# Optimization experiments

Measured on AMD Instinct MI355X. Metric: run time of the kernel, lower is better.

## Reference

```python
import math
import jax, jax.numpy as jnp
import numpy as np

LMAX = 2


def _cg_complex(j1, m1, j2, m2, j3, m3):
    # Standard (Racah) Clebsch-Gordan coefficient <j1 m1 j2 m2 | j3 m3> for integer l.
    if m1 + m2 != m3 or j3 < abs(j1 - j2) or j3 > j1 + j2:
        return 0.0
    f = math.factorial
    pre = math.sqrt((2 * j3 + 1) * f(j3 + j1 - j2) * f(j3 - j1 + j2) * f(j1 + j2 - j3) / f(j1 + j2 + j3 + 1))
    pre *= math.sqrt(f(j3 + m3) * f(j3 - m3) * f(j1 - m1) * f(j1 + m1) * f(j2 - m2) * f(j2 + m2))
    kmin = max(0, j2 - j3 - m1, j1 + m2 - j3)
    kmax = min(j1 + j2 - j3, j1 - m1, j2 + m2)
    s = 0.0
    for k in range(kmin, kmax + 1):
        s += (-1.0) ** k / (f(k) * f(j1 + j2 - j3 - k) * f(j1 - m1 - k) * f(j2 + m2 - k) * f(j3 - j2 + m1 + k) * f(j3 - j1 - m2 + k))
    return pre * s


def _u_matrix(l):
    # Unitary map from complex SH (Condon-Shortley) to real SH, rows = real mu, cols = complex m.
    U = np.zeros((2 * l + 1, 2 * l + 1), dtype=np.complex128)
    U[l, l] = 1.0
    isq2 = 1.0 / math.sqrt(2.0)
    for m in range(1, l + 1):
        U[l + m, l - m] = isq2
        U[l + m, l + m] = ((-1.0) ** m) * isq2
        U[l - m, l - m] = 1j * isq2
        U[l - m, l + m] = -1j * ((-1.0) ** m) * isq2
    return U


def _real_clebsch_gordan(lmax):
    # Dense real-SH CG tensor over combined s=(l,m) indices, shape [S,S,S], S=(lmax+1)^2.
    S = (lmax + 1) ** 2
    cg = np.zeros((S, S, S))
    for l1 in range(lmax + 1):
        for l2 in range(lmax + 1):
            for l3 in range(abs(l1 - l2), min(lmax, l1 + l2) + 1):
                blk = np.zeros((2 * l1 + 1, 2 * l2 + 1, 2 * l3 + 1))
                for i1, m1 in enumerate(range(-l1, l1 + 1)):
                    for i2, m2 in enumerate(range(-l2, l2 + 1)):
                        for i3, m3 in enumerate(range(-l3, l3 + 1)):
                            blk[i1, i2, i3] = _cg_complex(l1, m1, l2, m2, l3, m3)
                U1, U2, U3 = _u_matrix(l1), _u_matrix(l2), _u_matrix(l3)
                r = np.einsum('am,bn,co,mno->abc', U1, U2, U3.conj(), blk.astype(np.complex128))
                r = r.real if (l1 + l2 + l3) % 2 == 0 else r.imag  # parity-dependent real part
                cg[l1 * l1:(l1 + 1) ** 2, l2 * l2:(l2 + 1) ** 2, l3 * l3:(l3 + 1) ** 2] = r
    return cg


def _sparse_cg(lmax):
    cg = _real_clebsch_gordan(lmax)
    i1, i2, i3 = np.nonzero(np.abs(cg) > 1e-10)
    vals = cg[i1, i2, i3].astype(np.float32)
    widx = np.floor(np.sqrt(i3.astype(np.float64))).astype(np.int32)  # l of output combined index
    return vals, i1.astype(np.int32), i2.astype(np.int32), i3.astype(np.int32), widx


def _spherical_harmonics_l2(d):
    # Real SH up to l=2, 'component' normalization (|x|=1 assumed). Order: (l,m) = (0,0),(1,-1),(1,0),(1,1),(2,-2..2).
    x, y, z = d[..., 0], d[..., 1], d[..., 2]
    s3, s5, s15 = math.sqrt(3.0), math.sqrt(5.0), math.sqrt(15.0)
    return jnp.stack([
        jnp.ones_like(x),
        s3 * y, s3 * z, s3 * x,
        s15 * x * y, s15 * y * z, 0.5 * s5 * (3.0 * z * z - 1.0), s15 * x * z, 0.5 * s15 * (x * x - y * y),
    ], axis=-1)


def setup_inputs():
    N_ATOMS, N_EDGES, N_BASIS, N_RADIAL = 1200, 12000, 128, 20
    S = (LMAX + 1) ** 2
    key = jax.random.key(0)
    ks = jax.random.split(key, 8)
    vals, i1, i2, i3, widx = _sparse_cg(LMAX)
    return {
        'x': jax.random.normal(ks[0], (N_ATOMS, S, N_BASIS), jnp.float32),
        'radial_ij': jax.random.uniform(ks[1], (N_EDGES, N_RADIAL), jnp.float32),
        'dir_ij': jax.random.normal(ks[2], (N_EDGES, 3), jnp.float32),
        'cutoff_ij': jax.random.uniform(ks[3], (N_EDGES, 1), jnp.float32),
        'W_filter': jax.random.normal(ks[6], (N_RADIAL, N_BASIS * (LMAX + 1)), jnp.float32) / math.sqrt(N_RADIAL),
        'b_filter': jnp.zeros((N_BASIS * (LMAX + 1),), jnp.float32),
        'cg_vals': jnp.asarray(vals),
        'idx_i': jax.random.randint(ks[4], (N_EDGES,), 0, N_ATOMS),
        'idx_j': jax.random.randint(ks[5], (N_EDGES,), 0, N_ATOMS),
        'cg_idx_in1': jnp.asarray(i1),
        'cg_idx_in2': jnp.asarray(i2),
        'cg_idx_out': jnp.asarray(i3),
        'w_idx': jnp.asarray(widx),
    }


def reference(x, radial_ij, dir_ij, cutoff_ij, W_filter, b_filter, cg_vals,
              idx_i, idx_j, cg_idx_in1, cg_idx_in2, cg_idx_out, w_idx):
    n_atoms, S, F = x.shape
    E = dir_ij.shape[0]
    d = dir_ij / jnp.linalg.norm(dir_ij, axis=-1, keepdims=True)
    Y = _spherical_harmonics_l2(d)                        # [E, S]
    Wij = (radial_ij @ W_filter + b_filter) * cutoff_ij   # [E, (lmax+1)*F]
    Wij = Wij.reshape(E, LMAX + 1, F)                     # per-l radial filter
    xj = x[idx_j]                                         # [E, S, F] neighbor features
    # Sparse CG tensor-product contraction over combined (l,m) indices.
    v = (Y[:, cg_idx_in2, None] * cg_vals[None, :, None]
         * Wij[:, w_idx, :] * xj[:, cg_idx_in1, :])       # [E, n_cg, F]
    yij = jnp.zeros((E, S, F), v.dtype).at[:, cg_idx_out, :].add(v)
    return jax.ops.segment_sum(yij, idx_i, num_segments=n_atoms)
```

## Files before the change

kernel.cpp:

```cpp
#include <hip/hip_runtime.h>
#include <math.h>


#define S9     9
#define MROW   12
#define NF     128
#define NRAD   20
#define CEDGE  4
#define MAXA   2048

__device__ inline float2 f2fma(float a, float2 b, float2 c) {
    return make_float2(fmaf(a, b.x, c.x), fmaf(a, b.y, c.y));
}

__global__ __launch_bounds__(1024) void csr_kernel(
    const int* __restrict__ idx_i, int E, int A, int max_chunks,
    int* __restrict__ offsets,
    int* __restrict__ chunk_off,
    int* __restrict__ chunk_atom,
    int* __restrict__ esorted,
    float* __restrict__ out)
{
    __shared__ int lcnt[MAXA];
    __shared__ int lcur[MAXA];
    __shared__ unsigned long long wtot[16];
    __shared__ int nch_sh;
    const int t = threadIdx.x;
    const int lane = t & 63;
    const int wid  = t >> 6;

    for (int i = t; i < A; i += 1024) lcnt[i] = 0;
    __syncthreads();
    for (int e = t; e < E; e += 1024) atomicAdd(&lcnt[idx_i[e]], 1);
    __syncthreads();

    const int i0 = 2 * t, i1 = 2 * t + 1;
    const int ca = (i0 < A) ? lcnt[i0] : 0;
    const int cb = (i1 < A) ? lcnt[i1] : 0;
    const int ka = (i0 < A) ? ((ca + CEDGE - 1) / CEDGE) : 0;
    const int kb = (i1 < A) ? ((cb + CEDGE - 1) / CEDGE) : 0;

    const unsigned long long mine =
        (unsigned long long)(unsigned)(ca + cb) |
        ((unsigned long long)(unsigned)(ka + kb) << 32);
    unsigned long long inc = mine;
    #pragma unroll
    for (int d = 1; d < 64; d <<= 1) {
        unsigned long long u = __shfl_up(inc, d);
        if (lane >= d) inc += u;
    }
    if (lane == 63) wtot[wid] = inc;
    __syncthreads();
    if (wid == 0) {
        unsigned long long w = (lane < 16) ? wtot[lane] : 0ull;
        #pragma unroll
        for (int d = 1; d < 16; d <<= 1) {
            unsigned long long u = __shfl_up(w, d);
            if (lane >= d) w += u;
        }
        if (lane < 16) wtot[lane] = w;
    }
    __syncthreads();
    const unsigned long long wpre = (wid > 0) ? wtot[wid - 1] : 0ull;
    const unsigned long long exc  = wpre + (inc - mine);

    int run  = (int)(exc & 0xffffffffull);
    int run2 = (int)(exc >> 32);
    if (i0 < A) {
        offsets[i0] = run; lcur[i0] = run; chunk_off[i0] = run2;
        for (int k = 0; k < ka; ++k) chunk_atom[run2 + k] = i0;
        run += ca; run2 += ka;
    }
    if (i1 < A) {
        offsets[i1] = run; lcur[i1] = run; chunk_off[i1] = run2;
        for (int k = 0; k < kb; ++k) chunk_atom[run2 + k] = i1;
        run += cb; run2 += kb;
    }
    if (t == 1023) {
        const unsigned long long g = wtot[15];
        offsets[A]   = (int)(g & 0xffffffffull);
        chunk_off[A] = (int)(g >> 32);
        nch_sh       = (int)(g >> 32);
    }

    const float4 z4 = make_float4(0.f, 0.f, 0.f, 0.f);
    if (i0 < A && ca == 0) {
        float4* o = (float4*)(out + (size_t)i0 * (S9 * NF));
        for (int s = 0; s < S9 * NF / 4; ++s) o[s] = z4;
    }
    if (i1 < A && cb == 0) {
        float4* o = (float4*)(out + (size_t)i1 * (S9 * NF));
        for (int s = 0; s < S9 * NF / 4; ++s) o[s] = z4;
    }
    __syncthreads();

    for (int i = nch_sh + t; i < max_chunks; i += 1024) chunk_atom[i] = -1;

    for (int e = t; e < E; e += 1024) {
        int p = atomicAdd(&lcur[idx_i[e]], 1);
        esorted[p] = e;
    }
}

__global__ __launch_bounds__(64) void so3_chunk_kernel(
    const float* __restrict__ x,
    const float* __restrict__ radial,
    const float* __restrict__ dir,
    const float* __restrict__ cutoff,
    const float* __restrict__ Wf,
    const float* __restrict__ bf,
    const float* __restrict__ cg_vals,
    const int* __restrict__ idx_j,
    const int* __restrict__ cg_i1,
    const int* __restrict__ cg_i2,
    const int* __restrict__ cg_i3,
    int ncg, int A,
    const int* __restrict__ offsets,
    const int* __restrict__ chunk_off,
    const int* __restrict__ chunk_atom,
    const int* __restrict__ esorted,
    float* __restrict__ slots,
    float* __restrict__ out,
    int use_slots)
{
    const int ch = blockIdx.x;
    const int a = chunk_atom[ch];
    if (a < 0) return;

    const int c0ch = chunk_off[a];
    const int nch  = chunk_off[a + 1] - c0ch;
    const int estart = offsets[a] + (ch - c0ch) * CEDGE;
    const int n = min(CEDGE, offsets[a + 1] - estart);

    const int t = threadIdx.x;

    __shared__ __align__(16) float M[CEDGE][MROW * S9];
    __shared__ float Ysh[CEDGE][S9];
    __shared__ float radsh[CEDGE][NRAD];
    __shared__ float cutsh[CEDGE];
    __shared__ int   jsh[CEDGE];

    {
        float4* Mz = (float4*)&M[0][0];
        const int tot4 = CEDGE * MROW * S9 / 4;
        for (int qq = t; qq < tot4; qq += 64) Mz[qq] = make_float4(0.f, 0.f, 0.f, 0.f);
    }
    if (t < CEDGE) {
        int jj = a;
        float cut = 0.f;
        if (t < n) {
            const int e = esorted[estart + t];
            jj = idx_j[e];
            cut = cutoff[e];
            float dx = dir[3 * e], dy = dir[3 * e + 1], dz = dir[3 * e + 2];
            const float inv = rsqrtf(dx * dx + dy * dy + dz * dz);
            dx *= inv; dy *= inv; dz *= inv;
            const float s3c  = 1.7320508075688772f;
            const float s5c  = 2.2360679774997896f;
            const float s15c = 3.8729833462074170f;
            Ysh[t][0] = 1.0f;
            Ysh[t][1] = s3c * dy;
            Ysh[t][2] = s3c * dz;
            Ysh[t][3] = s3c * dx;
            Ysh[t][4] = s15c * dx * dy;
            Ysh[t][5] = s15c * dy * dz;
            Ysh[t][6] = 0.5f * s5c * (3.0f * dz * dz - 1.0f);
            Ysh[t][7] = s15c * dx * dz;
            Ysh[t][8] = 0.5f * s15c * (dx * dx - dy * dy);
        }
        jsh[t] = jj;
        cutsh[t] = cut;
    }
    for (int qq = t; qq < CEDGE * NRAD; qq += 64) {
        const int c = qq / NRAD;
        const int r = qq - c * NRAD;
        radsh[c][r] = (c < n) ? radial[(size_t)esorted[estart + c] * NRAD + r] : 0.f;
    }
    __syncthreads();

    float2 w[CEDGE][3];
    {
        const float2 b0 = ((const float2*)(bf + 0 * NF))[t];
        const float2 b1 = ((const float2*)(bf + 1 * NF))[t];
        const float2 b2 = ((const float2*)(bf + 2 * NF))[t];
        #pragma unroll
        for (int c = 0; c < CEDGE; ++c) { w[c][0] = b0; w[c][1] = b1; w[c][2] = b2; }
        #pragma unroll 4
        for (int r = 0; r < NRAD; ++r) {
            const float2* wrow = (const float2*)(Wf + r * (3 * NF));
            const float2 w0 = wrow[t];
            const float2 w1 = wrow[t + 64];
            const float2 w2 = wrow[t + 128];
            #pragma unroll
            for (int c = 0; c < CEDGE; ++c) {
                const float rv = radsh[c][r];
                w[c][0] = f2fma(rv, w0, w[c][0]);
                w[c][1] = f2fma(rv, w1, w[c][1]);
                w[c][2] = f2fma(rv, w2, w[c][2]);
            }
        }
        #pragma unroll
        for (int c = 0; c < CEDGE; ++c) {
            const float cut = cutsh[c];
            w[c][0].x *= cut; w[c][0].y *= cut;
            w[c][1].x *= cut; w[c][1].y *= cut;
            w[c][2].x *= cut; w[c][2].y *= cut;
        }
    }

    {
        const int c = t >> 4;
        const int r = t & 15;
        if (c < n) {
            for (int kk = r; kk < ncg; kk += 16) {
                atomicAdd(&M[c][cg_i3[kk] * MROW + cg_i1[kk]], cg_vals[kk] * Ysh[c][cg_i2[kk]]);
            }
        }
    }
    __syncthreads();

    float2 acc[S9];
    #pragma unroll
    for (int s = 0; s < S9; ++s) acc[s] = make_float2(0.f, 0.f);

    #pragma unroll
    for (int c = 0; c < CEDGE; ++c) {
        const int j = __builtin_amdgcn_readfirstlane(jsh[c]);

        const float2* xp = (const float2*)(x + (size_t)j * (S9 * NF)) + t;
        float2 xj[S9];
        #pragma unroll
        for (int s = 0; s < S9; ++s) xj[s] = xp[s * 64];

        #pragma unroll
        for (int s3 = 0; s3 < S9; ++s3) {
            const float4* mr = (const float4*)&M[c][s3 * MROW];
            const float4 m0 = mr[0];
            const float4 m1 = mr[1];
            const float  m8 = M[c][s3 * MROW + 8];
            float2 tsum = make_float2(0.f, 0.f);
            tsum = f2fma(m0.x, xj[0], tsum);
            tsum = f2fma(m0.y, xj[1], tsum);
            tsum = f2fma(m0.z, xj[2], tsum);
            tsum = f2fma(m0.w, xj[3], tsum);
            tsum = f2fma(m1.x, xj[4], tsum);
            tsum = f2fma(m1.y, xj[5], tsum);
            tsum = f2fma(m1.z, xj[6], tsum);
            tsum = f2fma(m1.w, xj[7], tsum);
            tsum = f2fma(m8,   xj[8], tsum);
            const float2 wl = (s3 == 0) ? w[c][0] : ((s3 < 4) ? w[c][1] : w[c][2]);
            acc[s3].x = fmaf(wl.x, tsum.x, acc[s3].x);
            acc[s3].y = fmaf(wl.y, tsum.y, acc[s3].y);
        }
    }

    if (!use_slots) {
        float* op = out + (size_t)a * (S9 * NF) + 2 * t;
        #pragma unroll
        for (int s = 0; s < S9; ++s) {
            atomicAdd(&op[s * NF],     acc[s].x);
            atomicAdd(&op[s * NF + 1], acc[s].y);
        }
        return;
    }

    if (nch == 1) {
        float2* op = (float2*)(out + (size_t)a * (S9 * NF)) + t;
        #pragma unroll
        for (int s = 0; s < S9; ++s) op[s * 64] = acc[s];
    } else {
        float2* sp = (float2*)(slots + (size_t)ch * (S9 * NF)) + t;
        #pragma unroll
        for (int s = 0; s < S9; ++s) sp[s * 64] = acc[s];
    }
}

__global__ __launch_bounds__(64) void so3_reduce_kernel(
    const float* __restrict__ slots, const int* __restrict__ chunk_off,
    float* __restrict__ out)
{
    const int a = blockIdx.x;
    const int t = threadIdx.x;
    const int c0 = chunk_off[a];
    const int c1 = chunk_off[a + 1];
    if (c1 - c0 < 2) return;

    float2 acc[S9];
    #pragma unroll
    for (int s = 0; s < S9; ++s) acc[s] = make_float2(0.f, 0.f);

    for (int ch = c0; ch < c1; ++ch) {
        const float2* sp = (const float2*)(slots + (size_t)ch * (S9 * NF)) + t;
        #pragma unroll
        for (int s = 0; s < S9; ++s) {
            float2 v = sp[s * 64];
            acc[s].x += v.x; acc[s].y += v.y;
        }
    }
    float2* op = (float2*)(out + (size_t)a * (S9 * NF)) + t;
    #pragma unroll
    for (int s = 0; s < S9; ++s) op[s * 64] = acc[s];
}

extern "C" void kernel_launch(void* const* d_in, const int* in_sizes, int n_in,
                              void* d_out, int out_size, void* d_ws, size_t ws_size,
                              hipStream_t stream) {
    const float* x       = (const float*)d_in[0];
    const float* radial  = (const float*)d_in[1];
    const float* dir     = (const float*)d_in[2];
    const float* cutoff  = (const float*)d_in[3];
    const float* Wf      = (const float*)d_in[4];
    const float* bf      = (const float*)d_in[5];
    const float* cg_vals = (const float*)d_in[6];
    const int*   idx_i   = (const int*)d_in[7];
    const int*   idx_j   = (const int*)d_in[8];
    const int*   cg_i1   = (const int*)d_in[9];
    const int*   cg_i2   = (const int*)d_in[10];
    const int*   cg_i3   = (const int*)d_in[11];

    const int E   = in_sizes[7];
    const int ncg = in_sizes[6];
    const int A   = in_sizes[0] / (S9 * NF);

    const int max_chunks = E / CEDGE + A;

    int* offsets    = (int*)d_ws;
    int* chunk_off  = offsets + (A + 1);
    int* chunk_atom = chunk_off + (A + 1);
    int* esorted    = chunk_atom + max_chunks;
    size_t int_bytes = (size_t)(2 * A + 2 + max_chunks + E) * sizeof(int);
    size_t slots_off = (int_bytes + 255) & ~(size_t)255;

    size_t slots_bytes = (size_t)max_chunks * (S9 * NF) * sizeof(float);
    const int use_slots = (ws_size >= slots_off + slots_bytes) ? 1 : 0;
    float* slots = (float*)((char*)d_ws + slots_off);
    float* out   = (float*)d_out;

    if (!use_slots) {
        hipMemsetAsync(out, 0, (size_t)out_size * sizeof(float), stream);
    }

    csr_kernel<<<1, 1024, 0, stream>>>(idx_i, E, A, max_chunks,
                                       offsets, chunk_off, chunk_atom, esorted, out);

    so3_chunk_kernel<<<max_chunks, 64, 0, stream>>>(
        x, radial, dir, cutoff, Wf, bf, cg_vals, idx_j,
        cg_i1, cg_i2, cg_i3, ncg, A, offsets, chunk_off, chunk_atom, esorted,
        slots, out, use_slots);

    if (use_slots) {
        so3_reduce_kernel<<<A, 64, 0, stream>>>(slots, chunk_off, out);
    }
}
```

Baseline: 124.5 us.

## Process all edges of an atom in one block, drop chunk slots and reduce pass

Replaces the per-chunk grid (4 edges per block, partial sums written to slots, then a separate reduce kernel) with one block per atom that loops over that atom's edges in tiles of 8 and writes the output directly. The CSR build is simplified to plain offsets, and the edge sort is staged in shared memory when E fits. This removes the slot traffic, the third kernel launch and the chunk bookkeeping. In exchange the grid shrinks to A blocks of 64 threads, so parallelism falls and atoms with many edges become serial tails.

```diff
diff --git a/kernel.cpp b/kernel.cpp
--- a/kernel.cpp
+++ b/kernel.cpp
@@ -6,25 +6,22 @@
 #define MROW   12
 #define NF     128
 #define NRAD   20
-#define CEDGE  4
+#define TEDGE  8
 #define MAXA   2048
+#define EMAX   12288
 
 __device__ inline float2 f2fma(float a, float2 b, float2 c) {
     return make_float2(fmaf(a, b.x, c.x), fmaf(a, b.y, c.y));
 }
 
 __global__ __launch_bounds__(1024) void csr_kernel(
-    const int* __restrict__ idx_i, int E, int A, int max_chunks,
+    const int* __restrict__ idx_i, int E, int A,
     int* __restrict__ offsets,
-    int* __restrict__ chunk_off,
-    int* __restrict__ chunk_atom,
-    int* __restrict__ esorted,
-    float* __restrict__ out)
+    int* __restrict__ esorted)
 {
     __shared__ int lcnt[MAXA];
-    __shared__ int lcur[MAXA];
-    __shared__ unsigned long long wtot[16];
-    __shared__ int nch_sh;
+    __shared__ int wtot[16];
+    __shared__ int esh[EMAX];
     const int t = threadIdx.x;
     const int lane = t & 63;
     const int wid  = t >> 6;
@@ -37,72 +34,48 @@
     const int i0 = 2 * t, i1 = 2 * t + 1;
     const int ca = (i0 < A) ? lcnt[i0] : 0;
     const int cb = (i1 < A) ? lcnt[i1] : 0;
-    const int ka = (i0 < A) ? ((ca + CEDGE - 1) / CEDGE) : 0;
-    const int kb = (i1 < A) ? ((cb + CEDGE - 1) / CEDGE) : 0;
-
-    const unsigned long long mine =
-        (unsigned long long)(unsigned)(ca + cb) |
-        ((unsigned long long)(unsigned)(ka + kb) << 32);
-    unsigned long long inc = mine;
+    __syncthreads();
+
+    int inc = ca + cb;
     #pragma unroll
     for (int d = 1; d < 64; d <<= 1) {
-        unsigned long long u = __shfl_up(inc, d);
+        int u = __shfl_up(inc, d);
         if (lane >= d) inc += u;
     }
     if (lane == 63) wtot[wid] = inc;
     __syncthreads();
     if (wid == 0) {
-        unsigned long long w = (lane < 16) ? wtot[lane] : 0ull;
+        int w = (lane < 16) ? wtot[lane] : 0;
         #pragma unroll
         for (int d = 1; d < 16; d <<= 1) {
-            unsigned long long u = __shfl_up(w, d);
+            int u = __shfl_up(w, d);
             if (lane >= d) w += u;
         }
         if (lane < 16) wtot[lane] = w;
     }
     __syncthreads();
-    const unsigned long long wpre = (wid > 0) ? wtot[wid - 1] : 0ull;
-    const unsigned long long exc  = wpre + (inc - mine);
-
-    int run  = (int)(exc & 0xffffffffull);
-    int run2 = (int)(exc >> 32);
-    if (i0 < A) {
-        offsets[i0] = run; lcur[i0] = run; chunk_off[i0] = run2;
-        for (int k = 0; k < ka; ++k) chunk_atom[run2 + k] = i0;
-        run += ca; run2 += ka;
-    }
-    if (i1 < A) {
-        offsets[i1] = run; lcur[i1] = run; chunk_off[i1] = run2;
-        for (int k = 0; k < kb; ++k) chunk_atom[run2 + k] = i1;
-        run += cb; run2 += kb;
-    }
-    if (t == 1023) {
-        const unsigned long long g = wtot[15];
-        offsets[A]   = (int)(g & 0xffffffffull);
-        chunk_off[A] = (int)(g >> 32);
-        nch_sh       = (int)(g >> 32);
-    }
-
-    const float4 z4 = make_float4(0.f, 0.f, 0.f, 0.f);
-    if (i0 < A && ca == 0) {
-        float4* o = (float4*)(out + (size_t)i0 * (S9 * NF));
-        for (int s = 0; s < S9 * NF / 4; ++s) o[s] = z4;
-    }
-    if (i1 < A && cb == 0) {
-        float4* o = (float4*)(out + (size_t)i1 * (S9 * NF));
-        for (int s = 0; s < S9 * NF / 4; ++s) o[s] = z4;
-    }
-    __syncthreads();
-
-    for (int i = nch_sh + t; i < max_chunks; i += 1024) chunk_atom[i] = -1;
-
-    for (int e = t; e < E; e += 1024) {
-        int p = atomicAdd(&lcur[idx_i[e]], 1);
-        esorted[p] = e;
-    }
-}
-
-__global__ __launch_bounds__(64) void so3_chunk_kernel(
+    int run = ((wid > 0) ? wtot[wid - 1] : 0) + (inc - (ca + cb));
+    if (i0 < A) { offsets[i0] = run; lcnt[i0] = run; run += ca; }
+    if (i1 < A) { offsets[i1] = run; lcnt[i1] = run; run += cb; }
+    if (t == 1023) offsets[A] = wtot[15];
+    __syncthreads();
+
+    if (E <= EMAX) {
+        for (int e = t; e < E; e += 1024) {
+            int p = atomicAdd(&lcnt[idx_i[e]], 1);
+            esh[p] = e;
+        }
+        __syncthreads();
+        for (int i = t; i < E; i += 1024) esorted[i] = esh[i];
+    } else {
+        for (int e = t; e < E; e += 1024) {
+            int p = atomicAdd(&lcnt[idx_i[e]], 1);
+            esorted[p] = e;
+        }
+    }
+}
+
+__global__ __launch_bounds__(64) void so3_atom_kernel(
     const float* __restrict__ x,
     const float* __restrict__ radial,
     const float* __restrict__ dir,
@@ -114,77 +87,74 @@
     const int* __restrict__ cg_i1,
     const int* __restrict__ cg_i2,
     const int* __restrict__ cg_i3,
-    int ncg, int A,
+    int ncg,
     const int* __restrict__ offsets,
-    const int* __restrict__ chunk_off,
-    const int* __restrict__ chunk_atom,
     const int* __restrict__ esorted,
-    float* __restrict__ slots,
-    float* __restrict__ out,
-    int use_slots)
+    float* __restrict__ out)
 {
-    const int ch = blockIdx.x;
-    const int a = chunk_atom[ch];
-    if (a < 0) return;
-
-    const int c0ch = chunk_off[a];
-    const int nch  = chunk_off[a + 1] - c0ch;
-    const int estart = offsets[a] + (ch - c0ch) * CEDGE;
-    const int n = min(CEDGE, offsets[a + 1] - estart);
-
+    const int a = blockIdx.x;
     const int t = threadIdx.x;
-
-    __shared__ __align__(16) float M[CEDGE][MROW * S9];
-    __shared__ float Ysh[CEDGE][S9];
-    __shared__ float radsh[CEDGE][NRAD];
-    __shared__ float cutsh[CEDGE];
-    __shared__ int   jsh[CEDGE];
-
-    {
-        float4* Mz = (float4*)&M[0][0];
-        const int tot4 = CEDGE * MROW * S9 / 4;
-        for (int qq = t; qq < tot4; qq += 64) Mz[qq] = make_float4(0.f, 0.f, 0.f, 0.f);
-    }
-    if (t < CEDGE) {
-        int jj = a;
-        float cut = 0.f;
-        if (t < n) {
-            const int e = esorted[estart + t];
-            jj = idx_j[e];
-            cut = cutoff[e];
-            float dx = dir[3 * e], dy = dir[3 * e + 1], dz = dir[3 * e + 2];
-            const float inv = rsqrtf(dx * dx + dy * dy + dz * dz);
-            dx *= inv; dy *= inv; dz *= inv;
-            const float s3c  = 1.7320508075688772f;
-            const float s5c  = 2.2360679774997896f;
-            const float s15c = 3.8729833462074170f;
-            Ysh[t][0] = 1.0f;
-            Ysh[t][1] = s3c * dy;
-            Ysh[t][2] = s3c * dz;
-            Ysh[t][3] = s3c * dx;
-            Ysh[t][4] = s15c * dx * dy;
-            Ysh[t][5] = s15c * dy * dz;
-            Ysh[t][6] = 0.5f * s5c * (3.0f * dz * dz - 1.0f);
-            Ysh[t][7] = s15c * dx * dz;
-            Ysh[t][8] = 0.5f * s15c * (dx * dx - dy * dy);
-        }
-        jsh[t] = jj;
-        cutsh[t] = cut;
-    }
-    for (int qq = t; qq < CEDGE * NRAD; qq += 64) {
-        const int c = qq / NRAD;
-        const int r = qq - c * NRAD;
-        radsh[c][r] = (c < n) ? radial[(size_t)esorted[estart + c] * NRAD + r] : 0.f;
-    }
-    __syncthreads();
-
-    float2 w[CEDGE][3];
-    {
-        const float2 b0 = ((const float2*)(bf + 0 * NF))[t];
-        const float2 b1 = ((const float2*)(bf + 1 * NF))[t];
-        const float2 b2 = ((const float2*)(bf + 2 * NF))[t];
-        #pragma unroll
-        for (int c = 0; c < CEDGE; ++c) { w[c][0] = b0; w[c][1] = b1; w[c][2] = b2; }
+    const int e0 = offsets[a];
+    const int e1 = offsets[a + 1];
+
+    __shared__ __align__(16) float M[TEDGE][MROW * S9];
+    __shared__ float Ysh[TEDGE][S9];
+    __shared__ float radsh[TEDGE][NRAD];
+    __shared__ float cutsh[TEDGE];
+    __shared__ int   jsh[TEDGE];
+
+    float2 acc[S9];
+    #pragma unroll
+    for (int s = 0; s < S9; ++s) acc[s] = make_float2(0.f, 0.f);
+
+    const float2 b0 = ((const float2*)(bf + 0 * NF))[t];
+    const float2 b1 = ((const float2*)(bf + 1 * NF))[t];
+    const float2 b2 = ((const float2*)(bf + 2 * NF))[t];
+
+    for (int base = e0; base < e1; base += TEDGE) {
+        const int n = min(TEDGE, e1 - base);
+
+        {
+            float4* Mz = (float4*)&M[0][0];
+            const int tot4 = TEDGE * MROW * S9 / 4;
+            for (int qq = t; qq < tot4; qq += 64) Mz[qq] = make_float4(0.f, 0.f, 0.f, 0.f);
+        }
+        if (t < TEDGE) {
+            int jj = a;
+            float cut = 0.f;
+            if (t < n) {
+                const int e = esorted[base + t];
+                jj = idx_j[e];
+                cut = cutoff[e];
+                float dx = dir[3 * e], dy = dir[3 * e + 1], dz = dir[3 * e + 2];
+                const float inv = rsqrtf(dx * dx + dy * dy + dz * dz);
+                dx *= inv; dy *= inv; dz *= inv;
+                const float s3c  = 1.7320508075688772f;
+                const float s5c  = 2.2360679774997896f;
+                const float s15c = 3.8729833462074170f;
+                Ysh[t][0] = 1.0f;
+                Ysh[t][1] = s3c * dy;
+                Ysh[t][2] = s3c * dz;
+                Ysh[t][3] = s3c * dx;
+                Ysh[t][4] = s15c * dx * dy;
+                Ysh[t][5] = s15c * dy * dz;
+                Ysh[t][6] = 0.5f * s5c * (3.0f * dz * dz - 1.0f);
+                Ysh[t][7] = s15c * dx * dz;
+                Ysh[t][8] = 0.5f * s15c * (dx * dx - dy * dy);
+            }
+            jsh[t] = jj;
+            cutsh[t] = cut;
+        }
+        for (int qq = t; qq < TEDGE * NRAD; qq += 64) {
+            const int c = qq / NRAD;
+            const int r = qq - c * NRAD;
+            radsh[c][r] = (c < n) ? radial[(size_t)esorted[base + c] * NRAD + r] : 0.f;
+        }
+        __syncthreads();
+
+        float2 w[TEDGE][3];
+        #pragma unroll
+        for (int c = 0; c < TEDGE; ++c) { w[c][0] = b0; w[c][1] = b1; w[c][2] = b2; }
         #pragma unroll 4
         for (int r = 0; r < NRAD; ++r) {
             const float2* wrow = (const float2*)(Wf + r * (3 * NF));
@@ -192,7 +162,7 @@
             const float2 w1 = wrow[t + 64];
             const float2 w2 = wrow[t + 128];
             #pragma unroll
-            for (int c = 0; c < CEDGE; ++c) {
+            for (int c = 0; c < TEDGE; ++c) {
                 const float rv = radsh[c][r];
                 w[c][0] = f2fma(rv, w0, w[c][0]);
                 w[c][1] = f2fma(rv, w1, w[c][1]);
@@ -200,103 +170,57 @@
             }
         }
         #pragma unroll
-        for (int c = 0; c < CEDGE; ++c) {
+        for (int c = 0; c < TEDGE; ++c) {
             const float cut = cutsh[c];
             w[c][0].x *= cut; w[c][0].y *= cut;
             w[c][1].x *= cut; w[c][1].y *= cut;
             w[c][2].x *= cut; w[c][2].y *= cut;
         }
-    }
-
-    {
-        const int c = t >> 4;
-        const int r = t & 15;
-        if (c < n) {
-            for (int kk = r; kk < ncg; kk += 16) {
-                atomicAdd(&M[c][cg_i3[kk] * MROW + cg_i1[kk]], cg_vals[kk] * Ysh[c][cg_i2[kk]]);
-            }
-        }
-    }
-    __syncthreads();
-
-    float2 acc[S9];
-    #pragma unroll
-    for (int s = 0; s < S9; ++s) acc[s] = make_float2(0.f, 0.f);
-
-    #pragma unroll
-    for (int c = 0; c < CEDGE; ++c) {
-        const int j = __builtin_amdgcn_readfirstlane(jsh[c]);
-
-        const float2* xp = (const float2*)(x + (size_t)j * (S9 * NF)) + t;
-        float2 xj[S9];
-        #pragma unroll
-        for (int s = 0; s < S9; ++s) xj[s] = xp[s * 64];
-
-        #pragma unroll
-        for (int s3 = 0; s3 < S9; ++s3) {
-            const float4* mr = (const float4*)&M[c][s3 * MROW];
-            const float4 m0 = mr[0];
-            const float4 m1 = mr[1];
-            const float  m8 = M[c][s3 * MROW + 8];
-            float2 tsum = make_float2(0.f, 0.f);
-            tsum = f2fma(m0.x, xj[0], tsum);
-            tsum = f2fma(m0.y, xj[1], tsum);
-            tsum = f2fma(m0.z, xj[2], tsum);
-            tsum = f2fma(m0.w, xj[3], tsum);
-            tsum = f2fma(m1.x, xj[4], tsum);
-            tsum = f2fma(m1.y, xj[5], tsum);
-            tsum = f2fma(m1.z, xj[6], tsum);
-            tsum = f2fma(m1.w, xj[7], tsum);
-            tsum = f2fma(m8,   xj[8], tsum);
-            const float2 wl = (s3 == 0) ? w[c][0] : ((s3 < 4) ? w[c][1] : w[c][2]);
-            acc[s3].x = fmaf(wl.x, tsum.x, acc[s3].x);
-            acc[s3].y = fmaf(wl.y, tsum.y, acc[s3].y);
-        }
-    }
-
-    if (!use_slots) {
-        float* op = out + (size_t)a * (S9 * NF) + 2 * t;
-        #pragma unroll
-        for (int s = 0; s < S9; ++s) {
-            atomicAdd(&op[s * NF],     acc[s].x);
-            atomicAdd(&op[s * NF + 1], acc[s].y);
-        }
-        return;
-    }
-
-    if (nch == 1) {
-        float2* op = (float2*)(out + (size_t)a * (S9 * NF)) + t;
-        #pragma unroll
-        for (int s = 0; s < S9; ++s) op[s * 64] = acc[s];
-    } else {
-        float2* sp = (float2*)(slots + (size_t)ch * (S9 * NF)) + t;
-        #pragma unroll
-        for (int s = 0; s < S9; ++s) sp[s * 64] = acc[s];
-    }
-}
-
-__global__ __launch_bounds__(64) void so3_reduce_kernel(
-    const float* __restrict__ slots, const int* __restrict__ chunk_off,
-    float* __restrict__ out)
-{
-    const int a = blockIdx.x;
-    const int t = threadIdx.x;
-    const int c0 = chunk_off[a];
-    const int c1 = chunk_off[a + 1];
-    if (c1 - c0 < 2) return;
-
-    float2 acc[S9];
-    #pragma unroll
-    for (int s = 0; s < S9; ++s) acc[s] = make_float2(0.f, 0.f);
-
-    for (int ch = c0; ch < c1; ++ch) {
-        const float2* sp = (const float2*)(slots + (size_t)ch * (S9 * NF)) + t;
-        #pragma unroll
-        for (int s = 0; s < S9; ++s) {
-            float2 v = sp[s * 64];
-            acc[s].x += v.x; acc[s].y += v.y;
-        }
-    }
+
+        {
+            const int c = t >> 3;
+            const int r = t & 7;
+            if (c < n) {
+                for (int kk = r; kk < ncg; kk += 8) {
+                    atomicAdd(&M[c][cg_i3[kk] * MROW + cg_i1[kk]], cg_vals[kk] * Ysh[c][cg_i2[kk]]);
+                }
+            }
+        }
+        __syncthreads();
+
+        #pragma unroll
+        for (int c = 0; c < TEDGE; ++c) {
+            const int j = __builtin_amdgcn_readfirstlane(jsh[c]);
+
+            const float2* xp = (const float2*)(x + (size_t)j * (S9 * NF)) + t;
+            float2 xj[S9];
+            #pragma unroll
+            for (int s = 0; s < S9; ++s) xj[s] = xp[s * 64];
+
+            #pragma unroll
+            for (int s3 = 0; s3 < S9; ++s3) {
+                const float4* mr = (const float4*)&M[c][s3 * MROW];
+                const float4 m0 = mr[0];
+                const float4 m1 = mr[1];
+                const float  m8 = M[c][s3 * MROW + 8];
+                float2 tsum = make_float2(0.f, 0.f);
+                tsum = f2fma(m0.x, xj[0], tsum);
+                tsum = f2fma(m0.y, xj[1], tsum);
+                tsum = f2fma(m0.z, xj[2], tsum);
+                tsum = f2fma(m0.w, xj[3], tsum);
+                tsum = f2fma(m1.x, xj[4], tsum);
+                tsum = f2fma(m1.y, xj[5], tsum);
+                tsum = f2fma(m1.z, xj[6], tsum);
+                tsum = f2fma(m1.w, xj[7], tsum);
+                tsum = f2fma(m8,   xj[8], tsum);
+                const float2 wl = (s3 == 0) ? w[c][0] : ((s3 < 4) ? w[c][1] : w[c][2]);
+                acc[s3].x = fmaf(wl.x, tsum.x, acc[s3].x);
+                acc[s3].y = fmaf(wl.y, tsum.y, acc[s3].y);
+            }
+        }
+        __syncthreads();
+    }
+
     float2* op = (float2*)(out + (size_t)a * (S9 * NF)) + t;
     #pragma unroll
     for (int s = 0; s < S9; ++s) op[s * 64] = acc[s];
@@ -322,33 +246,12 @@
     const int ncg = in_sizes[6];
     const int A   = in_sizes[0] / (S9 * NF);
 
-    const int max_chunks = E / CEDGE + A;
-
-    int* offsets    = (int*)d_ws;
-    int* chunk_off  = offsets + (A + 1);
-    int* chunk_atom = chunk_off + (A + 1);
-    int* esorted    = chunk_atom + max_chunks;
-    size_t int_bytes = (size_t)(2 * A + 2 + max_chunks + E) * sizeof(int);
-    size_t slots_off = (int_bytes + 255) & ~(size_t)255;
-
-    size_t slots_bytes = (size_t)max_chunks * (S9 * NF) * sizeof(float);
-    const int use_slots = (ws_size >= slots_off + slots_bytes) ? 1 : 0;
-    float* slots = (float*)((char*)d_ws + slots_off);
-    float* out   = (float*)d_out;
-
-    if (!use_slots) {
-        hipMemsetAsync(out, 0, (size_t)out_size * sizeof(float), stream);
-    }
-
-    csr_kernel<<<1, 1024, 0, stream>>>(idx_i, E, A, max_chunks,
-                                       offsets, chunk_off, chunk_atom, esorted, out);
-
-    so3_chunk_kernel<<<max_chunks, 64, 0, stream>>>(
+    int* offsets = (int*)d_ws;
+    int* esorted = offsets + (A + 1);
+
+    csr_kernel<<<1, 1024, 0, stream>>>(idx_i, E, A, offsets, esorted);
+
+    so3_atom_kernel<<<A, 64, 0, stream>>>(
         x, radial, dir, cutoff, Wf, bf, cg_vals, idx_j,
-        cg_i1, cg_i2, cg_i3, ncg, A, offsets, chunk_off, chunk_atom, esorted,
-        slots, out, use_slots);
-
-    if (use_slots) {
-        so3_reduce_kernel<<<A, 64, 0, stream>>>(slots, chunk_off, out);
-    }
-}
+        cg_i1, cg_i2, cg_i3, ncg, offsets, esorted, (float*)d_out);
+}
```

New measurement: 137.3 us. 1.1x slower.
